# Kernel optimization log

Hardware: AMD Instinct MI355X
Metric: run time of the kernel (lower is better)

The kernel has to match this reference:

```python
import jax, jax.numpy as jnp
import numpy as np

ALPHA = 1.0  # init alpha


def setup_inputs() -> dict:
    key = jax.random.key(0)
    X = jax.random.normal(key, (4096, 512), dtype=jnp.float32)
    return {"X": X}


def reference(X):
    # Pairwise squared L2 distances via GEMM expansion:
    # ||x_i - x_j||^2 = ||x_i||^2 + ||x_j||^2 - 2 x_i . x_j
    # (same math as ((X[None]-X[:,None])**2).sum(-1) without the O(N^2 D) blow-up)
    sq = jnp.sum(X * X, axis=1)                      # [N]
    d2 = sq[:, None] + sq[None, :] - 2.0 * (X @ X.T)  # [N, N]
    # track_running_stats=True: sigma^2 = alpha * mean(d2), detached in torch
    sigma_square = ALPHA * jax.lax.stop_gradient(jnp.mean(d2))
    return jnp.exp(-d2 / (2.0 * sigma_square))
```

## Files before the change

kernel.cpp:

```cpp
#include <hip/hip_runtime.h>
#include <cstdint>

typedef unsigned short u16;
typedef unsigned int u32;
typedef __bf16 bf16x8 __attribute__((ext_vector_type(8)));
typedef float f32x4 __attribute__((ext_vector_type(4)));

#define N_ROWS 4096
#define D_COLS 512

__device__ __forceinline__ u16 f2bf(float f) {
    u32 u = __float_as_uint(f);
    u += 0x7fffu + ((u >> 16) & 1u);
    return (u16)(u >> 16);
}

#define GLDS(g, l)                                                            \
    __builtin_amdgcn_global_load_lds(                                         \
        (const __attribute__((address_space(1))) void*)(g),                   \
        (__attribute__((address_space(3))) void*)(l), 16, 0, 0)

__global__ __launch_bounds__(256) void k_prep(const float* __restrict__ X,
                                              u16* __restrict__ Xb,
                                              float* __restrict__ sq,
                                              float* __restrict__ partial) {
    __shared__ float cs[4][512];
    const int tid = threadIdx.x;
    const int w = tid >> 6, l = tid & 63;
    const int row0 = blockIdx.x * 16 + w * 4;
    float csum[8] = {0.f,0.f,0.f,0.f,0.f,0.f,0.f,0.f};
#pragma unroll
    for (int r = 0; r < 4; ++r) {
        const int row = row0 + r;
        const float4* src = (const float4*)(X + (size_t)row * D_COLS);
        float4 f0 = src[l * 2];
        float4 f1 = src[l * 2 + 1];
        float v[8] = {f0.x, f0.y, f0.z, f0.w, f1.x, f1.y, f1.z, f1.w};
        float ss = 0.f;
#pragma unroll
        for (int j = 0; j < 8; ++j) { ss += v[j] * v[j]; csum[j] += v[j]; }
        uint4 st;
        st.x = (u32)f2bf(v[0]) | ((u32)f2bf(v[1]) << 16);
        st.y = (u32)f2bf(v[2]) | ((u32)f2bf(v[3]) << 16);
        st.z = (u32)f2bf(v[4]) | ((u32)f2bf(v[5]) << 16);
        st.w = (u32)f2bf(v[6]) | ((u32)f2bf(v[7]) << 16);
        *(uint4*)(Xb + (size_t)row * D_COLS + l * 8) = st;
#pragma unroll
        for (int m = 32; m > 0; m >>= 1) ss += __shfl_xor(ss, m, 64);
        if (l == 0) sq[row] = ss;
    }
#pragma unroll
    for (int j = 0; j < 8; ++j) cs[w][l * 8 + j] = csum[j];
    __syncthreads();
    for (int d = tid; d < 512; d += 256)
        partial[blockIdx.x * 512 + d] = cs[0][d] + cs[1][d] + cs[2][d] + cs[3][d];
}

__global__ __launch_bounds__(1024) void k_sigma(const float* __restrict__ sq,
                                                const float* __restrict__ partial,
                                                float* __restrict__ cout) {
    __shared__ float red[1024];
    const int t = threadIdx.x;
    float s1 = sq[t] + sq[t + 1024] + sq[t + 2048] + sq[t + 3072];
    float s2 = 0.f;
    if (t < 512) {
        float s = 0.f;
#pragma unroll 8
        for (int b = 0; b < 256; ++b) s += partial[b * 512 + t];
        s2 = s * s;
    }
    red[t] = s1; __syncthreads();
    for (int st = 512; st > 0; st >>= 1) { if (t < st) red[t] += red[t + st]; __syncthreads(); }
    const float S1 = red[0]; __syncthreads();
    red[t] = s2; __syncthreads();
    for (int st = 512; st > 0; st >>= 1) { if (t < st) red[t] += red[t + st]; __syncthreads(); }
    if (t == 0) {
        const float S2 = red[0];
        const float mean_d2 = 2.f * S1 / (float)N_ROWS
                            - 2.f * S2 / ((float)N_ROWS * (float)N_ROWS);
        const float sigma2 = 1.0f * mean_d2;
        cout[0] = -1.4426950408889634f / (2.f * sigma2);
    }
}

__global__ __launch_bounds__(512, 2) void k_gemm(const u16* __restrict__ Xb,
                                                 const float* __restrict__ sq,
                                                 const float* __restrict__ cptr,
                                                 float* __restrict__ out) {
    __shared__ u16 As[2][256 * 64];
    __shared__ u16 Bs[2][256 * 64];
    __shared__ float sqA[256], sqB[256];

    const int tid = threadIdx.x;
    const int lane = tid & 63;
    const int wid = tid >> 6;
    const int wr = wid >> 2, wc = wid & 3;
    const int i0 = blockIdx.y * 256;
    const int j0 = blockIdx.x * 256;
    const float cval = cptr[0];

    if (tid < 256) sqA[tid] = sq[i0 + tid];
    else           sqB[tid - 256] = sq[j0 + tid - 256];

    const int srow = tid >> 3;
    const int scb = (tid & 7) * 16;
    const int ssw = scb ^ ((srow & 7) << 4);
    const char* xb = (const char*)Xb;
    const char* pA = xb + (size_t)(i0 + srow) * 1024 + ssw;
    const char* pB = xb + (size_t)(j0 + srow) * 1024 + ssw;

#define STAGE(buf, kt)                                                        \
    do {                                                                      \
        _Pragma("unroll")                                                     \
        for (int g = 0; g < 4; ++g) {                                         \
            GLDS(pA + (size_t)g * 65536 + (kt) * 128,                         \
                 (char*)As[buf] + g * 8192 + tid * 16);                       \
            GLDS(pB + (size_t)g * 65536 + (kt) * 128,                         \
                 (char*)Bs[buf] + g * 8192 + tid * 16);                       \
        }                                                                     \
    } while (0)

    f32x4 acc[8][4];
#pragma unroll
    for (int m = 0; m < 8; ++m)
#pragma unroll
        for (int n = 0; n < 4; ++n) acc[m][n] = (f32x4){0.f, 0.f, 0.f, 0.f};

    const int frow = lane & 15;
    const int klane = lane >> 4;
    const int swz = (frow & 7) << 4;

    STAGE(0, 0);
    __syncthreads();

    int cur = 0;
    for (int kt = 0; kt < 8; ++kt) {
        if (kt < 7) {
            if (cur == 0) STAGE(1, kt + 1); else STAGE(0, kt + 1);
        }
#pragma unroll
        for (int ks = 0; ks < 2; ++ks) {
            bf16x8 a[8], b[4];
            const int kb = (ks * 64 + klane * 16) ^ swz;
#pragma unroll
            for (int m = 0; m < 8; ++m)
                a[m] = *(const bf16x8*)((const char*)As[cur] +
                                        (wr * 128 + m * 16 + frow) * 128 + kb);
#pragma unroll
            for (int n = 0; n < 4; ++n)
                b[n] = *(const bf16x8*)((const char*)Bs[cur] +
                                        (wc * 64 + n * 16 + frow) * 128 + kb);
#pragma unroll
            for (int m = 0; m < 8; ++m)
#pragma unroll
                for (int n = 0; n < 4; ++n)
                    acc[m][n] = __builtin_amdgcn_mfma_f32_16x16x32_bf16(
                        a[m], b[n], acc[m][n], 0, 0, 0);
        }
        __syncthreads();
        cur ^= 1;
    }

    const int q = lane >> 4;
#pragma unroll
    for (int m = 0; m < 8; ++m) {
#pragma unroll
        for (int n = 0; n < 4; ++n) {
            const int col = wc * 64 + n * 16 + frow;
            const float sb = sqB[col];
#pragma unroll
            for (int r = 0; r < 4; ++r) {
                const int row = wr * 128 + m * 16 + q * 4 + r;
                const float d2 = sqA[row] + sb - 2.0f * acc[m][n][r];
                out[(size_t)(i0 + row) * N_ROWS + (j0 + col)] = exp2f(cval * d2);
            }
        }
    }
#undef STAGE
}

extern "C" void kernel_launch(void* const* d_in, const int* in_sizes, int n_in,
                              void* d_out, int out_size, void* d_ws, size_t ws_size,
                              hipStream_t stream) {
    const float* X = (const float*)d_in[0];
    float* out = (float*)d_out;
    char* ws = (char*)d_ws;

    u16*   Xb   = (u16*)ws;
    float* part = (float*)(ws + (4u << 20));
    float* sq   = (float*)(ws + (4u << 20) + (512u << 10));
    float* cptr = (float*)(ws + (4u << 20) + (512u << 10) + (16u << 10));

    hipLaunchKernelGGL(k_prep, dim3(256), dim3(256), 0, stream, X, Xb, sq, part);
    hipLaunchKernelGGL(k_sigma, dim3(1), dim3(1024), 0, stream, sq, part, cptr);
    hipLaunchKernelGGL(k_gemm, dim3(16, 16), dim3(512), 0, stream, Xb, sq, cptr, out);
}
```

Baseline: 53.24 us.

## Triple-buffer GEMM K-loop, parallelize sigma reduction, remap tiles across XCDs

Replaces the single-block sigma reduction with 8 blocks producing partial sums, and folds the final sigma computation into the GEMM prologue. The GEMM now uses three LDS stages of K=32 with explicit vmcnt waits and a single barrier per step, so more global loads are in flight. It also boosts wave priority during MFMA issue and remaps the flat block index so neighbouring tiles share an XCD's L2. The cost is more loop iterations and more barriers, since the K step is smaller.

```diff
diff --git a/kernel.cpp b/kernel.cpp
--- a/kernel.cpp
+++ b/kernel.cpp
@@ -56,68 +56,85 @@
         partial[blockIdx.x * 512 + d] = cs[0][d] + cs[1][d] + cs[2][d] + cs[3][d];
 }
 
-__global__ __launch_bounds__(1024) void k_sigma(const float* __restrict__ sq,
-                                                const float* __restrict__ partial,
-                                                float* __restrict__ cout) {
-    __shared__ float red[1024];
+__global__ __launch_bounds__(256) void k_sigma(const float* __restrict__ sq,
+                                               const float* __restrict__ partial,
+                                               float* __restrict__ parts) {
+    __shared__ float csm[4][64];
+    __shared__ float red[8];
+    const int g = blockIdx.x;
     const int t = threadIdx.x;
-    float s1 = sq[t] + sq[t + 1024] + sq[t + 2048] + sq[t + 3072];
+    const int c = g * 64 + (t & 63);
+    const int ch = t >> 6;
+    float cssum = 0.f;
+#pragma unroll 8
+    for (int b = ch * 64; b < ch * 64 + 64; ++b) cssum += partial[b * 512 + c];
+    csm[ch][t & 63] = cssum;
+    float s1 = sq[g * 512 + t] + sq[g * 512 + 256 + t];
+    __syncthreads();
     float s2 = 0.f;
-    if (t < 512) {
-        float s = 0.f;
-#pragma unroll 8
-        for (int b = 0; b < 256; ++b) s += partial[b * 512 + t];
-        s2 = s * s;
-    }
-    red[t] = s1; __syncthreads();
-    for (int st = 512; st > 0; st >>= 1) { if (t < st) red[t] += red[t + st]; __syncthreads(); }
-    const float S1 = red[0]; __syncthreads();
-    red[t] = s2; __syncthreads();
-    for (int st = 512; st > 0; st >>= 1) { if (t < st) red[t] += red[t + st]; __syncthreads(); }
+    if (t < 64) {
+        float v = csm[0][t] + csm[1][t] + csm[2][t] + csm[3][t];
+        s2 = v * v;
+    }
+#pragma unroll
+    for (int m = 32; m > 0; m >>= 1) {
+        s1 += __shfl_xor(s1, m, 64);
+        s2 += __shfl_xor(s2, m, 64);
+    }
+    if ((t & 63) == 0) { red[ch] = s1; red[4 + ch] = s2; }
+    __syncthreads();
     if (t == 0) {
-        const float S2 = red[0];
-        const float mean_d2 = 2.f * S1 / (float)N_ROWS
-                            - 2.f * S2 / ((float)N_ROWS * (float)N_ROWS);
-        const float sigma2 = 1.0f * mean_d2;
-        cout[0] = -1.4426950408889634f / (2.f * sigma2);
+        parts[g] = red[0] + red[1] + red[2] + red[3];
+        parts[8 + g] = red[4];
     }
 }
 
 __global__ __launch_bounds__(512, 2) void k_gemm(const u16* __restrict__ Xb,
                                                  const float* __restrict__ sq,
-                                                 const float* __restrict__ cptr,
+                                                 const float* __restrict__ parts,
                                                  float* __restrict__ out) {
-    __shared__ u16 As[2][256 * 64];
-    __shared__ u16 Bs[2][256 * 64];
+    __shared__ __align__(16) u16 As[3][256 * 32];
+    __shared__ __align__(16) u16 Bs[3][256 * 32];
     __shared__ float sqA[256], sqB[256];
+    __shared__ float c_sh;
 
     const int tid = threadIdx.x;
     const int lane = tid & 63;
     const int wid = tid >> 6;
     const int wr = wid >> 2, wc = wid & 3;
-    const int i0 = blockIdx.y * 256;
-    const int j0 = blockIdx.x * 256;
-    const float cval = cptr[0];
+
+    const int bid = blockIdx.x;
+    const int xcd = bid & 7, rr = bid >> 3;
+    const int by = (xcd >> 2) * 8 + (rr & 7);
+    const int bx = (xcd & 3) * 4 + (rr >> 3);
+    const int i0 = by * 256, j0 = bx * 256;
 
     if (tid < 256) sqA[tid] = sq[i0 + tid];
     else           sqB[tid - 256] = sq[j0 + tid - 256];
-
-    const int srow = tid >> 3;
-    const int scb = (tid & 7) * 16;
-    const int ssw = scb ^ ((srow & 7) << 4);
+    if (tid == 0) {
+        float S1 = 0.f, S2 = 0.f;
+#pragma unroll
+        for (int i = 0; i < 8; ++i) { S1 += parts[i]; S2 += parts[8 + i]; }
+        const float mean_d2 = 2.f * S1 / (float)N_ROWS
+                            - 2.f * S2 / ((float)N_ROWS * (float)N_ROWS);
+        c_sh = -1.4426950408889634f / (2.f * mean_d2);
+    }
+
+    const int srow = tid >> 2;
+    const int sby = (tid & 3) * 16;
+    const int ssw = sby ^ ((srow & 3) << 4);
     const char* xb = (const char*)Xb;
-    const char* pA = xb + (size_t)(i0 + srow) * 1024 + ssw;
-    const char* pB = xb + (size_t)(j0 + srow) * 1024 + ssw;
+    const char* gA0 = xb + (size_t)(i0 + srow) * 1024 + ssw;
+    const char* gA1 = xb + (size_t)(i0 + srow + 128) * 1024 + ssw;
+    const char* gB0 = xb + (size_t)(j0 + srow) * 1024 + ssw;
+    const char* gB1 = xb + (size_t)(j0 + srow + 128) * 1024 + ssw;
 
 #define STAGE(buf, kt)                                                        \
     do {                                                                      \
-        _Pragma("unroll")                                                     \
-        for (int g = 0; g < 4; ++g) {                                         \
-            GLDS(pA + (size_t)g * 65536 + (kt) * 128,                         \
-                 (char*)As[buf] + g * 8192 + tid * 16);                       \
-            GLDS(pB + (size_t)g * 65536 + (kt) * 128,                         \
-                 (char*)Bs[buf] + g * 8192 + tid * 16);                       \
-        }                                                                     \
+        GLDS(gA0 + (kt) * 64, (char*)As[buf] + tid * 16);                     \
+        GLDS(gA1 + (kt) * 64, (char*)As[buf] + 8192 + tid * 16);              \
+        GLDS(gB0 + (kt) * 64, (char*)Bs[buf] + tid * 16);                     \
+        GLDS(gB1 + (kt) * 64, (char*)Bs[buf] + 8192 + tid * 16);              \
     } while (0)
 
     f32x4 acc[8][4];
@@ -128,39 +145,40 @@
 
     const int frow = lane & 15;
     const int klane = lane >> 4;
-    const int swz = (frow & 7) << 4;
+    const int asw = (klane * 16) ^ ((frow & 3) << 4);
+    const int abase = (wr * 128 + frow) * 64 + asw;
+    const int bbase = (wc * 64 + frow) * 64 + asw;
 
     STAGE(0, 0);
-    __syncthreads();
-
-    int cur = 0;
-    for (int kt = 0; kt < 8; ++kt) {
-        if (kt < 7) {
-            if (cur == 0) STAGE(1, kt + 1); else STAGE(0, kt + 1);
-        }
-#pragma unroll
-        for (int ks = 0; ks < 2; ++ks) {
-            bf16x8 a[8], b[4];
-            const int kb = (ks * 64 + klane * 16) ^ swz;
-#pragma unroll
-            for (int m = 0; m < 8; ++m)
-                a[m] = *(const bf16x8*)((const char*)As[cur] +
-                                        (wr * 128 + m * 16 + frow) * 128 + kb);
+    STAGE(1, 1);
+
+    int cb = 0, nb = 2;
+    for (int kt = 0; kt < 16; ++kt) {
+        if (kt < 15) asm volatile("s_waitcnt vmcnt(4)" ::: "memory");
+        else         asm volatile("s_waitcnt vmcnt(0)" ::: "memory");
+        asm volatile("s_barrier" ::: "memory");
+        if (kt + 2 < 16) STAGE(nb, kt + 2);
+        const char* Ab = (const char*)As[cb];
+        const char* Bb = (const char*)Bs[cb];
+        bf16x8 a[8], b[4];
+#pragma unroll
+        for (int m = 0; m < 8; ++m) a[m] = *(const bf16x8*)(Ab + abase + m * 1024);
+#pragma unroll
+        for (int n = 0; n < 4; ++n) b[n] = *(const bf16x8*)(Bb + bbase + n * 1024);
+        __builtin_amdgcn_s_setprio(1);
+#pragma unroll
+        for (int m = 0; m < 8; ++m)
 #pragma unroll
             for (int n = 0; n < 4; ++n)
-                b[n] = *(const bf16x8*)((const char*)Bs[cur] +
-                                        (wc * 64 + n * 16 + frow) * 128 + kb);
-#pragma unroll
-            for (int m = 0; m < 8; ++m)
-#pragma unroll
-                for (int n = 0; n < 4; ++n)
-                    acc[m][n] = __builtin_amdgcn_mfma_f32_16x16x32_bf16(
-                        a[m], b[n], acc[m][n], 0, 0, 0);
-        }
-        __syncthreads();
-        cur ^= 1;
-    }
-
+                acc[m][n] = __builtin_amdgcn_mfma_f32_16x16x32_bf16(
+                    a[m], b[n], acc[m][n], 0, 0, 0);
+        __builtin_amdgcn_s_setprio(0);
+        cb = (cb == 2) ? 0 : cb + 1;
+        nb = (nb == 2) ? 0 : nb + 1;
+    }
+#undef STAGE
+
+    const float cval = c_sh;
     const int q = lane >> 4;
 #pragma unroll
     for (int m = 0; m < 8; ++m) {
@@ -176,7 +194,6 @@
             }
         }
     }
-#undef STAGE
 }
 
 extern "C" void kernel_launch(void* const* d_in, const int* in_sizes, int n_in,
@@ -189,9 +206,9 @@
     u16*   Xb   = (u16*)ws;
     float* part = (float*)(ws + (4u << 20));
     float* sq   = (float*)(ws + (4u << 20) + (512u << 10));
-    float* cptr = (float*)(ws + (4u << 20) + (512u << 10) + (16u << 10));
+    float* prt  = (float*)(ws + (4u << 20) + (512u << 10) + (16u << 10));
 
     hipLaunchKernelGGL(k_prep, dim3(256), dim3(256), 0, stream, X, Xb, sq, part);
-    hipLaunchKernelGGL(k_sigma, dim3(1), dim3(1024), 0, stream, sq, part, cptr);
-    hipLaunchKernelGGL(k_gemm, dim3(16, 16), dim3(512), 0, stream, Xb, sq, cptr, out);
-}
+    hipLaunchKernelGGL(k_sigma, dim3(8), dim3(256), 0, stream, sq, part, prt);
+    hipLaunchKernelGGL(k_gemm, dim3(256), dim3(512), 0, stream, Xb, sq, prt, out);
+}
```

Measured after the change: 45.83 us. -13.9%, faster.
